# Performance work log

Hardware: AMD Instinct MI355X
Metric: run time of the kernel (lower is better)

The kernel has to match this reference:

```python
import jax, jax.numpy as jnp
import numpy as np

N = 50000
E = 800000
FEAT, ACT = 96, 32
HID, HEADS = 64, 4
NEG_SLOPE = 0.2


def gat_conv(x, src, dst, W, att_s, att_d, bias):
    # x: [N, F_in]; W: [F_in, H*C]; att_s/att_d: [H, C]; bias: [H*C]
    H, C = att_s.shape
    h = (x @ W).reshape(-1, H, C)                      # [N, H, C]
    a_s = jnp.einsum('nhc,hc->nh', h, att_s)           # [N, H]
    a_d = jnp.einsum('nhc,hc->nh', h, att_d)
    e = jax.nn.leaky_relu(a_s[src] + a_d[dst], NEG_SLOPE)  # [E, H]
    m = jax.ops.segment_max(e, dst, num_segments=N)
    e = jnp.exp(e - m[dst])
    denom = jax.ops.segment_sum(e, dst, num_segments=N)
    alpha = e / (denom[dst] + 1e-16)                   # softmax over incoming edges
    out = jax.ops.segment_sum(alpha[:, :, None] * h[src], dst, num_segments=N)
    return out.reshape(-1, H * C) + bias


def setup_inputs() -> dict:
    key = jax.random.key(0)
    ks = jax.random.split(key, 12)
    node_features = jax.random.normal(ks[0], (N, FEAT), dtype=jnp.float32)
    actions = jax.random.normal(ks[1], (N, ACT), dtype=jnp.float32)
    edge_index = jax.random.randint(ks[2], (2, E), 0, N, dtype=jnp.int64)
    s = 0.1
    return {
        'node_features': node_features,
        'actions': actions,
        'edge_index': edge_index,
        'W_emb': jax.random.normal(ks[3], (FEAT + ACT, HID), dtype=jnp.float32) * s,
        'b_emb': jnp.zeros((HID,), dtype=jnp.float32),
        'W1': jax.random.normal(ks[4], (HID, HEADS * HID), dtype=jnp.float32) * s,
        'att_s1': jax.random.normal(ks[5], (HEADS, HID), dtype=jnp.float32) * s,
        'att_d1': jax.random.normal(ks[6], (HEADS, HID), dtype=jnp.float32) * s,
        'b1': jnp.zeros((HEADS * HID,), dtype=jnp.float32),
        'W2': jax.random.normal(ks[7], (HEADS * HID, HID), dtype=jnp.float32) * s,
        'att_s2': jax.random.normal(ks[8], (1, HID), dtype=jnp.float32) * s,
        'att_d2': jax.random.normal(ks[9], (1, HID), dtype=jnp.float32) * s,
        'b2': jnp.zeros((HID,), dtype=jnp.float32),
        'W_v': jax.random.normal(ks[10], (HID, 1), dtype=jnp.float32) * s,
        'b_v': jnp.zeros((1,), dtype=jnp.float32),
    }


def reference(node_features, actions, edge_index, W_emb, b_emb, W1, att_s1, att_d1, b1,
              W2, att_s2, att_d2, b2, W_v, b_v):
    # add self loops (PyG GATConv default add_self_loops=True)
    loop = jnp.arange(N, dtype=edge_index.dtype)
    src = jnp.concatenate([edge_index[0], loop])
    dst = jnp.concatenate([edge_index[1], loop])
    x = jnp.concatenate([node_features, actions], axis=1)
    x = x @ W_emb + b_emb
    x = jax.nn.relu(gat_conv(x, src, dst, W1, att_s1, att_d1, b1))
    x = jax.nn.relu(gat_conv(x, src, dst, W2, att_s2, att_d2, b2))
    g = jnp.mean(x, axis=0, keepdims=True)  # [1, HID]
    return g @ W_v + b_v                    # [1, 1]
```

## Files before the change

kernel.cpp:

```cpp
#include <hip/hip_runtime.h>
#include <hip/hip_bf16.h>
#include <math.h>

#define FEAT 96
#define ACTF 32

using frag8 = __attribute__((ext_vector_type(8))) short;
using f32x4 = __attribute__((ext_vector_type(4))) float;

__device__ __forceinline__ float lrelu(float x) { return x >= 0.f ? x : 0.2f * x; }
__device__ __forceinline__ void atomAddF(float* p, float v) {
    __hip_atomic_fetch_add(p, v, __ATOMIC_RELAXED, __HIP_MEMORY_SCOPE_AGENT);
}
__device__ __forceinline__ float expc(float x) { return __expf(fminf(x, 60.f)); }
__device__ __forceinline__ unsigned short f2bf(float f) {
    __hip_bfloat16 h = __float2bfloat16(f);
    return *(unsigned short*)&h;
}
__device__ __forceinline__ float bf2f(unsigned short u) {
    return __uint_as_float((unsigned)u << 16);
}
__device__ __forceinline__ float bflo(unsigned u) { return __uint_as_float(u << 16); }
__device__ __forceinline__ float bfhi(unsigned u) { return __uint_as_float(u & 0xffff0000u); }

__global__ __launch_bounds__(256) void prep_all(
    const float* __restrict__ nf, const float* __restrict__ act,
    unsigned short* __restrict__ Xh, unsigned short* __restrict__ Xl,
    long long xtot, int xb,
    const float* __restrict__ Wemb, const float* __restrict__ bemb,
    const float* __restrict__ W1,
    unsigned short* __restrict__ wfh, unsigned short* __restrict__ wfl,
    float* __restrict__ bfused,
    const float* __restrict__ W2, __hip_bfloat16* __restrict__ w2t) {
    int b = blockIdx.x;
    if (b < xb) {
        long long i = (long long)b * 256 + threadIdx.x;
        if (i < xtot) {
            int n = (int)(i >> 7), k = (int)(i & 127);
            float v = (k < FEAT) ? nf[(size_t)n * FEAT + k] : act[(size_t)n * ACTF + (k - FEAT)];
            unsigned short h = f2bf(v);
            Xh[i] = h;
            Xl[i] = f2bf(v - bf2f(h));
        }
        return;
    }
    b -= xb;
    if (b < 129) {
        int k = b, c = threadIdx.x;
        if (k < 128) {
            float s = 0.f;
            for (int j = 0; j < 64; ++j) s = fmaf(Wemb[k * 64 + j], W1[j * 256 + c], s);
            unsigned short h = f2bf(s);
            wfh[(size_t)c * 128 + k] = h;
            wfl[(size_t)c * 128 + k] = f2bf(s - bf2f(h));
        } else {
            float s = 0.f;
            for (int j = 0; j < 64; ++j) s = fmaf(bemb[j], W1[j * 256 + c], s);
            bfused[c] = s;
        }
        return;
    }
    b -= 129;
    int i = b * 256 + threadIdx.x;
    int k = i >> 6, c = i & 63;
    w2t[(size_t)c * 256 + k] = __float2bfloat16(W2[i]);
}

__global__ __launch_bounds__(256, 2) void gemm1_hist(
    const unsigned short* __restrict__ Xh, const unsigned short* __restrict__ Xl,
    const unsigned short* __restrict__ wfh, const unsigned short* __restrict__ wfl,
    const float* __restrict__ bfused, const float* __restrict__ att_s,
    const float* __restrict__ att_d, __hip_bfloat16* __restrict__ h1b,
    float* __restrict__ a_s, float* __restrict__ a_d, int N,
    const int* __restrict__ dstp, int* __restrict__ cnt, int E, int ET, int gb) {
    if (blockIdx.x >= gb) {
        int e = (blockIdx.x - gb) * 256 + threadIdx.x;
        if (e < ET) {
            int d = (e < E) ? dstp[e] : (e - E);
            atomicAdd(&cnt[d], 1);
        }
        return;
    }
    int w = threadIdx.x >> 6, l = threadIdx.x & 63;
    int r16 = l & 15, kg = l >> 4;
    frag8 bh[4][4], bl[4][4];
    #pragma unroll
    for (int c = 0; c < 4; ++c) {
        int ct = w * 4 + c;
        const short* bhp = (const short*)wfh + (size_t)(ct * 16 + r16) * 128 + kg * 8;
        const short* blp = (const short*)wfl + (size_t)(ct * 16 + r16) * 128 + kg * 8;
        #pragma unroll
        for (int ks = 0; ks < 4; ++ks) {
            bh[c][ks] = *(const frag8*)(bhp + ks * 32);
            bl[c][ks] = *(const frag8*)(blp + ks * 32);
        }
    }
    float biasv[4], awv[4], dwv[4];
    #pragma unroll
    for (int c = 0; c < 4; ++c) {
        int ch = w * 64 + c * 16 + r16;
        biasv[c] = bfused[ch];
        awv[c] = att_s[ch];
        dwv[c] = att_d[ch];
    }
    int ntiles = (N + 15) >> 4;
    for (int tile = blockIdx.x; tile < ntiles; tile += gb) {
        int nb = tile * 16;
        int arow = nb + r16; if (arow >= N) arow = N - 1;
        const short* ahp = (const short*)Xh + (size_t)arow * 128 + kg * 8;
        const short* alp = (const short*)Xl + (size_t)arow * 128 + kg * 8;
        frag8 ah[4], al[4];
        #pragma unroll
        for (int ks = 0; ks < 4; ++ks) {
            ah[ks] = *(const frag8*)(ahp + ks * 32);
            al[ks] = *(const frag8*)(alp + ks * 32);
        }
        float s_s[4] = {0.f, 0.f, 0.f, 0.f}, s_d[4] = {0.f, 0.f, 0.f, 0.f};
        #pragma unroll
        for (int c = 0; c < 4; ++c) {
            f32x4 acc = (f32x4){0.f, 0.f, 0.f, 0.f};
            #pragma unroll
            for (int ks = 0; ks < 4; ++ks) {
                acc = __builtin_amdgcn_mfma_f32_16x16x32_bf16(ah[ks], bh[c][ks], acc, 0, 0, 0);
                acc = __builtin_amdgcn_mfma_f32_16x16x32_bf16(al[ks], bh[c][ks], acc, 0, 0, 0);
                acc = __builtin_amdgcn_mfma_f32_16x16x32_bf16(ah[ks], bl[c][ks], acc, 0, 0, 0);
            }
            int ch = w * 64 + c * 16 + r16;
            #pragma unroll
            for (int r = 0; r < 4; ++r) {
                int node = nb + kg * 4 + r;
                float v = acc[r] + biasv[c];
                if (node < N) h1b[(size_t)node * 256 + ch] = __float2bfloat16(v);
                s_s[r] = fmaf(v, awv[c], s_s[r]);
                s_d[r] = fmaf(v, dwv[c], s_d[r]);
            }
        }
        #pragma unroll
        for (int r = 0; r < 4; ++r) {
            float vs = s_s[r], vd = s_d[r];
            #pragma unroll
            for (int o = 1; o < 16; o <<= 1) {
                vs += __shfl_xor(vs, o);
                vd += __shfl_xor(vd, o);
            }
            int node = nb + kg * 4 + r;
            if (r16 == 0 && node < N) {
                a_s[(size_t)node * 4 + w] = vs;
                a_d[(size_t)node * 4 + w] = vd;
            }
        }
    }
}

__global__ __launch_bounds__(256, 2) void gemm2_mfma_w(
    const __hip_bfloat16* __restrict__ out1b, const __hip_bfloat16* __restrict__ w2t,
    const float* __restrict__ att_s, const float* __restrict__ att_d,
    __hip_bfloat16* __restrict__ h2b, float* __restrict__ a_s, float* __restrict__ a_d,
    int N) {
    int w = threadIdx.x >> 6, l = threadIdx.x & 63;
    int r16 = l & 15, kg = l >> 4;
    const short* B = (const short*)w2t;
    frag8 b[4][8];
    #pragma unroll
    for (int ct = 0; ct < 4; ++ct) {
        const short* brp = B + (size_t)(ct * 16 + r16) * 256 + kg * 8;
        #pragma unroll
        for (int ks = 0; ks < 8; ++ks)
            b[ct][ks] = *(const frag8*)(brp + ks * 32);
    }
    float awv[4], dwv[4];
    #pragma unroll
    for (int ct = 0; ct < 4; ++ct) {
        int ch = ct * 16 + r16;
        awv[ct] = att_s[ch];
        dwv[ct] = att_d[ch];
    }
    const short* A = (const short*)out1b;
    int ntiles = (N + 15) >> 4;
    for (int tile = blockIdx.x * 4 + w; tile < ntiles; tile += gridDim.x * 4) {
        int nb = tile * 16;
        int arow = nb + r16; if (arow >= N) arow = N - 1;
        const short* arp = A + (size_t)arow * 256 + kg * 8;
        frag8 a[8];
        #pragma unroll
        for (int ks = 0; ks < 8; ++ks) a[ks] = *(const frag8*)(arp + ks * 32);
        float s_s[4] = {0.f, 0.f, 0.f, 0.f}, s_d[4] = {0.f, 0.f, 0.f, 0.f};
        #pragma unroll
        for (int ct = 0; ct < 4; ++ct) {
            f32x4 acc = (f32x4){0.f, 0.f, 0.f, 0.f};
            #pragma unroll
            for (int ks = 0; ks < 8; ++ks)
                acc = __builtin_amdgcn_mfma_f32_16x16x32_bf16(a[ks], b[ct][ks], acc, 0, 0, 0);
            int ch = ct * 16 + r16;
            #pragma unroll
            for (int r = 0; r < 4; ++r) {
                int node = nb + kg * 4 + r;
                float v = acc[r];
                if (node < N) h2b[(size_t)node * 64 + ch] = __float2bfloat16(v);
                s_s[r] = fmaf(v, awv[ct], s_s[r]);
                s_d[r] = fmaf(v, dwv[ct], s_d[r]);
            }
        }
        #pragma unroll
        for (int r = 0; r < 4; ++r) {
            #pragma unroll
            for (int o = 1; o < 16; o <<= 1) {
                s_s[r] += __shfl_xor(s_s[r], o);
                s_d[r] += __shfl_xor(s_d[r], o);
            }
            int node = nb + kg * 4 + r;
            if (r16 == 0 && node < N) { a_s[node] = s_s[r]; a_d[node] = s_d[r]; }
        }
    }
}

__global__ __launch_bounds__(256) void scan_blocks(
    const int* __restrict__ cnt, int* __restrict__ offl, int* __restrict__ bsum, int n) {
    int b = blockIdx.x, t = threadIdx.x;
    int i = b * 256 + t;
    int v = (i < n) ? cnt[i] : 0;
    int lane = t & 63, w = t >> 6;
    int x = v;
    #pragma unroll
    for (int o = 1; o < 64; o <<= 1) {
        int y = __shfl_up(x, o);
        if (lane >= o) x += y;
    }
    __shared__ int wtot[4];
    if (lane == 63) wtot[w] = x;
    __syncthreads();
    int add = 0;
    #pragma unroll
    for (int j = 0; j < 4; ++j) if (j < w) add += wtot[j];
    int incl = x + add;
    if (i < n) offl[i] = incl - v;
    if (t == 255) bsum[b] = incl;
}

__global__ __launch_bounds__(256) void scan_tops(
    const int* __restrict__ bsum, int* __restrict__ bpre, int nb,
    float* __restrict__ g, int* __restrict__ done) {
    int t = threadIdx.x;
    int v = (t < nb) ? bsum[t] : 0;
    int lane = t & 63, w = t >> 6;
    int x = v;
    #pragma unroll
    for (int o = 1; o < 64; o <<= 1) {
        int y = __shfl_up(x, o);
        if (lane >= o) x += y;
    }
    __shared__ int wtot[4];
    if (lane == 63) wtot[w] = x;
    __syncthreads();
    int add = 0;
    #pragma unroll
    for (int j = 0; j < 4; ++j) if (j < w) add += wtot[j];
    if (t < nb) bpre[t] = x + add - v;
    if (t == 255) bpre[nb] = x + add;
    if (t < 64) g[t] = 0.f;
    if (t == 64) *done = 0;
}

__global__ void scatter_fin(const int* __restrict__ src, const int* __restrict__ dst,
                            const int* __restrict__ offl, const int* __restrict__ bpre,
                            int* __restrict__ cur, int* __restrict__ perm,
                            int* __restrict__ off, int E, int ET, int n, int nb, int sb) {
    if (blockIdx.x < sb) {
        int e = blockIdx.x * 256 + threadIdx.x;
        if (e >= ET) return;
        int s = (e < E) ? src[e] : (e - E);
        int d = (e < E) ? dst[e] : (e - E);
        int r = atomicAdd(&cur[d], 1);
        perm[offl[d] + bpre[d >> 8] + r] = s;
    } else {
        int i = (blockIdx.x - sb) * 256 + threadIdx.x;
        if (i < n) off[i] = offl[i] + bpre[i >> 8];
        if (i == n) off[n] = bpre[nb];
    }
}

__global__ __launch_bounds__(256) void fused_gat4(
    const int* __restrict__ off, const int* __restrict__ perm,
    const float* __restrict__ a_s, const float* __restrict__ a_d,
    const __hip_bfloat16* __restrict__ h1b, const float* __restrict__ bias,
    __hip_bfloat16* __restrict__ out1b, int N) {
    __shared__ float exls[4][4][68];
    __shared__ unsigned idxls[4][64];
    int w = threadIdx.x >> 6, l = threadIdx.x & 63;
    int d = blockIdx.x * 4 + w;
    if (d >= N) return;
    int lo = off[d], hi = off[d + 1];
    const float4* as4 = (const float4*)a_s;
    float4 ad = ((const float4*)a_d)[d];
    int eg = l >> 5;
    int li = l & 31;
    int gh = li >> 3;
    const char* hb = (const char*)h1b;
    unsigned laneoff = (unsigned)li * 16u;
    float acc[8] = {0.f, 0.f, 0.f, 0.f, 0.f, 0.f, 0.f, 0.f};
    float dx = 0.f, dy = 0.f, dz = 0.f, dw = 0.f;
    for (int base = lo; base < hi; base += 64) {
        int e = base + l;
        bool valid = e < hi;
        int s = valid ? perm[e] : 0;
        float4 a = as4[s];
        float e0 = valid ? expc(lrelu(a.x + ad.x)) : 0.f;
        float e1 = valid ? expc(lrelu(a.y + ad.y)) : 0.f;
        float e2 = valid ? expc(lrelu(a.z + ad.z)) : 0.f;
        float e3 = valid ? expc(lrelu(a.w + ad.w)) : 0.f;
        dx += e0; dy += e1; dz += e2; dw += e3;
        exls[w][0][l] = e0;
        exls[w][1][l] = e1;
        exls[w][2][l] = e2;
        exls[w][3][l] = e3;
        idxls[w][l] = valid ? (unsigned)s * 512u : 0u;
        int n = min(64, hi - base);
        #pragma unroll 2
        for (int i = 0; i < n; i += 2) {
            int ii = i + eg;
            float ex = exls[w][gh][ii];
            unsigned voff = idxls[w][ii] + laneoff;
            uint4 v = *(const uint4*)(hb + voff);
            acc[0] = fmaf(ex, bflo(v.x), acc[0]);
            acc[1] = fmaf(ex, bfhi(v.x), acc[1]);
            acc[2] = fmaf(ex, bflo(v.y), acc[2]);
            acc[3] = fmaf(ex, bfhi(v.y), acc[3]);
            acc[4] = fmaf(ex, bflo(v.z), acc[4]);
            acc[5] = fmaf(ex, bfhi(v.z), acc[5]);
            acc[6] = fmaf(ex, bflo(v.w), acc[6]);
            acc[7] = fmaf(ex, bfhi(v.w), acc[7]);
        }
    }
    #pragma unroll
    for (int o = 32; o; o >>= 1) {
        dx += __shfl_xor(dx, o); dy += __shfl_xor(dy, o);
        dz += __shfl_xor(dz, o); dw += __shfl_xor(dw, o);
    }
    float rr = 1.f / ((gh == 0 ? dx : gh == 1 ? dy : gh == 2 ? dz : dw) + 1e-16f);
    #pragma unroll
    for (int j = 0; j < 8; ++j) acc[j] += __shfl_xor(acc[j], 32);
    if (eg == 0) {
        float4 b0 = ((const float4*)bias)[li * 2];
        float4 b1 = ((const float4*)bias)[li * 2 + 1];
        uint4 pk;
        pk.x = (unsigned)f2bf(fmaxf(fmaf(acc[0], rr, b0.x), 0.f))
             | ((unsigned)f2bf(fmaxf(fmaf(acc[1], rr, b0.y), 0.f)) << 16);
        pk.y = (unsigned)f2bf(fmaxf(fmaf(acc[2], rr, b0.z), 0.f))
             | ((unsigned)f2bf(fmaxf(fmaf(acc[3], rr, b0.w), 0.f)) << 16);
        pk.z = (unsigned)f2bf(fmaxf(fmaf(acc[4], rr, b1.x), 0.f))
             | ((unsigned)f2bf(fmaxf(fmaf(acc[5], rr, b1.y), 0.f)) << 16);
        pk.w = (unsigned)f2bf(fmaxf(fmaf(acc[6], rr, b1.z), 0.f))
             | ((unsigned)f2bf(fmaxf(fmaf(acc[7], rr, b1.w), 0.f)) << 16);
        ((uint4*)(out1b + (size_t)d * 256))[li] = pk;
    }
}

__global__ __launch_bounds__(256) void fused_gat1(
    const int* __restrict__ off, const int* __restrict__ perm,
    const float* __restrict__ a_s, const float* __restrict__ a_d,
    const __hip_bfloat16* __restrict__ h2b, const float* __restrict__ bias,
    float* __restrict__ out2, int N) {
    __shared__ float exls1[4][64];
    __shared__ unsigned idxls1[4][64];
    int w = threadIdx.x >> 6, l = threadIdx.x & 63;
    int d = blockIdx.x * 4 + w;
    if (d >= N) return;
    int lo = off[d], hi = off[d + 1];
    float add = a_d[d];
    int eg = l >> 4;
    int li = l & 15;
    const char* hb = (const char*)h2b;
    unsigned laneoff = (unsigned)li * 8u;
    float den = 0.f;
    float acc0 = 0.f, acc1 = 0.f, acc2 = 0.f, acc3 = 0.f;
    for (int base = lo; base < hi; base += 64) {
        int e = base + l;
        bool valid = e < hi;
        int s = valid ? perm[e] : 0;
        float ex = valid ? expc(lrelu(a_s[s] + add)) : 0.f;
        den += ex;
        exls1[w][l] = ex;
        idxls1[w][l] = valid ? (unsigned)s * 128u : 0u;
        int n = min(64, hi - base);
        #pragma unroll 4
        for (int i = 0; i < n; i += 4) {
            int ii = i + eg;
            float exx = exls1[w][ii];
            unsigned voff = idxls1[w][ii] + laneoff;
            uint2 v = *(const uint2*)(hb + voff);
            acc0 = fmaf(exx, bflo(v.x), acc0);
            acc1 = fmaf(exx, bfhi(v.x), acc1);
            acc2 = fmaf(exx, bflo(v.y), acc2);
            acc3 = fmaf(exx, bfhi(v.y), acc3);
        }
    }
    #pragma unroll
    for (int o = 32; o; o >>= 1) den += __shfl_xor(den, o);
    float rr = 1.f / (den + 1e-16f);
    #pragma unroll
    for (int o = 16; o < 64; o <<= 1) {
        acc0 += __shfl_xor(acc0, o);
        acc1 += __shfl_xor(acc1, o);
        acc2 += __shfl_xor(acc2, o);
        acc3 += __shfl_xor(acc3, o);
    }
    if (eg == 0 && (l >> 4) == 0) {
        const float4* b4 = (const float4*)bias;
        float4 bv = b4[li];
        float4 o4;
        o4.x = fmaxf(fmaf(acc0, rr, bv.x), 0.f);
        o4.y = fmaxf(fmaf(acc1, rr, bv.y), 0.f);
        o4.z = fmaxf(fmaf(acc2, rr, bv.z), 0.f);
        o4.w = fmaxf(fmaf(acc3, rr, bv.w), 0.f);
        ((float4*)(out2 + (size_t)d * 64))[li] = o4;
    }
}

__global__ __launch_bounds__(256) void colsum_final(
    const float* __restrict__ x, float* __restrict__ g, int* __restrict__ done,
    const float* __restrict__ Wv, const float* __restrict__ bv,
    float* __restrict__ out, int N) {
    __shared__ float part[4][64];
    __shared__ int amlast;
    int c = threadIdx.x & 63;
    int r = threadIdx.x >> 6;
    float acc = 0.f;
    for (long long n = (long long)blockIdx.x * 4 + r; n < N; n += (long long)gridDim.x * 4)
        acc += x[n * 64 + c];
    part[r][c] = acc;
    __syncthreads();
    if (r == 0) {
        float v = part[0][c] + part[1][c] + part[2][c] + part[3][c];
        atomAddF(&g[c], v);
    }
    __threadfence();
    if (threadIdx.x == 0) {
        int t = __hip_atomic_fetch_add(done, 1, __ATOMIC_ACQ_REL, __HIP_MEMORY_SCOPE_AGENT);
        amlast = (t == (int)gridDim.x - 1) ? 1 : 0;
    }
    __syncthreads();
    if (amlast && threadIdx.x < 64) {
        float gc = __hip_atomic_load(&g[threadIdx.x], __ATOMIC_RELAXED, __HIP_MEMORY_SCOPE_AGENT);
        float v = (gc / (float)N) * Wv[threadIdx.x];
        #pragma unroll
        for (int o = 32; o; o >>= 1) v += __shfl_down(v, o);
        if (threadIdx.x == 0) out[0] = v + bv[0];
    }
}

extern "C" void kernel_launch(void* const* d_in, const int* in_sizes, int n_in,
                              void* d_out, int out_size, void* d_ws, size_t ws_size,
                              hipStream_t stream) {
    const float* nf   = (const float*)d_in[0];
    const float* act  = (const float*)d_in[1];
    const int*   ei   = (const int*)d_in[2];
    const float* Wemb = (const float*)d_in[3];
    const float* bemb = (const float*)d_in[4];
    const float* W1   = (const float*)d_in[5];
    const float* as1  = (const float*)d_in[6];
    const float* ad1  = (const float*)d_in[7];
    const float* b1   = (const float*)d_in[8];
    const float* W2   = (const float*)d_in[9];
    const float* as2  = (const float*)d_in[10];
    const float* ad2  = (const float*)d_in[11];
    const float* b2   = (const float*)d_in[12];
    const float* Wv   = (const float*)d_in[13];
    const float* bv   = (const float*)d_in[14];
    float* out = (float*)d_out;

    const int N = in_sizes[0] / FEAT;
    const int E = in_sizes[2] / 2;
    const int ET = E + N;
    const int* srcp = ei;
    const int* dstp = ei + E;
    const int NB = (N + 255) / 256;
    const int HB = (ET + 255) / 256;

    char* ws = (char*)d_ws;
    unsigned short* Xh = (unsigned short*)ws;
    unsigned short* Xl = Xh + (size_t)N * 128;
    __hip_bfloat16* h1b   = (__hip_bfloat16*)(Xl + (size_t)N * 128);
    __hip_bfloat16* out1b = h1b + (size_t)N * 256;
    float* a_s  = (float*)(out1b + (size_t)N * 256);
    float* a_d  = a_s + (size_t)N * 4;
    __hip_bfloat16* h2b = (__hip_bfloat16*)(a_d + (size_t)N * 4);
    float* out2 = (float*)(h2b + (size_t)N * 64);
    float* g    = out2 + (size_t)N * 64;
    __hip_bfloat16* w2t = (__hip_bfloat16*)(g + 64);
    unsigned short* wfh = (unsigned short*)(w2t + 64 * 256);
    unsigned short* wfl = wfh + 256 * 128;
    float* bfused = (float*)(wfl + 256 * 128);
    int* cnt  = (int*)(bfused + 256);
    int* cur  = cnt + N;
    int* offl = cur + N;
    int* off  = offl + N;
    int* perm = off + N + 1;
    int* bsum = perm + ET;
    int* bpre = bsum + NB;
    int* done = bpre + NB + 1;

    (void)ws_size; (void)n_in; (void)out_size;

    hipMemsetAsync(cnt, 0, (size_t)2 * N * sizeof(int), stream);

    long long xtot = (long long)N * 128;
    const int XB = (int)((xtot + 255) / 256);
    prep_all<<<XB + 129 + 64, 256, 0, stream>>>(nf, act, Xh, Xl, xtot, XB,
                                                Wemb, bemb, W1, wfh, wfl, bfused,
                                                W2, w2t);

    const int GB = 1024;
    gemm1_hist<<<GB + HB, 256, 0, stream>>>(Xh, Xl, wfh, wfl, bfused,
                                            as1, ad1, h1b, a_s, a_d, N,
                                            dstp, cnt, E, ET, GB);

    scan_blocks<<<NB, 256, 0, stream>>>(cnt, offl, bsum, N);
    scan_tops<<<1, 256, 0, stream>>>(bsum, bpre, NB, g, done);
    {
        const int FB = (N + 1 + 255) / 256;
        scatter_fin<<<HB + FB, 256, 0, stream>>>(srcp, dstp, offl, bpre, cur,
                                                 perm, off, E, ET, N, NB, HB);
    }

    fused_gat4<<<(N + 3) / 4, 256, 0, stream>>>(off, perm, a_s, a_d, h1b, b1, out1b, N);

    gemm2_mfma_w<<<512, 256, 0, stream>>>(out1b, w2t, as2, ad2, h2b, a_s, a_d, N);
    fused_gat1<<<(N + 3) / 4, 256, 0, stream>>>(off, perm, a_s, a_d, h2b, b2, out2, N);

    colsum_final<<<512, 256, 0, stream>>>(out2, g, done, Wv, bv, out, N);
}
```

Before: 286.4 us.

## Vectorize input bf16 split, prefetch next A tile, split histogram from GEMM1

The input prep now has each thread load 8 floats with float4 reads and write packed uint4 hi/lo bf16 values, replacing scalar per-element loads and stores. GEMM1 software-prefetches the next tile's A fragments into registers while computing the current tile, to hide global load latency. The destination histogram moves out of the fused GEMM kernel into its own launch. That adds one kernel launch and loses any overlap between the two, and the prefetch raises register pressure under launch_bounds(256,2).

```diff
diff --git a/kernel.cpp b/kernel.cpp
--- a/kernel.cpp
+++ b/kernel.cpp
@@ -26,7 +26,7 @@
 __global__ __launch_bounds__(256) void prep_all(
     const float* __restrict__ nf, const float* __restrict__ act,
     unsigned short* __restrict__ Xh, unsigned short* __restrict__ Xl,
-    long long xtot, int xb,
+    int N, int xb,
     const float* __restrict__ Wemb, const float* __restrict__ bemb,
     const float* __restrict__ W1,
     unsigned short* __restrict__ wfh, unsigned short* __restrict__ wfl,
@@ -34,13 +34,34 @@
     const float* __restrict__ W2, __hip_bfloat16* __restrict__ w2t) {
     int b = blockIdx.x;
     if (b < xb) {
-        long long i = (long long)b * 256 + threadIdx.x;
-        if (i < xtot) {
-            int n = (int)(i >> 7), k = (int)(i & 127);
-            float v = (k < FEAT) ? nf[(size_t)n * FEAT + k] : act[(size_t)n * ACTF + (k - FEAT)];
-            unsigned short h = f2bf(v);
-            Xh[i] = h;
-            Xl[i] = f2bf(v - bf2f(h));
+        int gid = b * 256 + threadIdx.x;
+        int node = gid >> 4, sub = gid & 15;
+        if (node < N) {
+            int k0 = sub * 8;
+            float4 v0, v1;
+            if (k0 < FEAT) {
+                const float4* p = (const float4*)(nf + (size_t)node * FEAT + k0);
+                v0 = p[0]; v1 = p[1];
+            } else {
+                const float4* p = (const float4*)(act + (size_t)node * ACTF + (k0 - FEAT));
+                v0 = p[0]; v1 = p[1];
+            }
+            float vv[8] = {v0.x, v0.y, v0.z, v0.w, v1.x, v1.y, v1.z, v1.w};
+            uint4 ph, pl;
+            unsigned hs[8], ls[8];
+            #pragma unroll
+            for (int j = 0; j < 8; ++j) {
+                unsigned short h = f2bf(vv[j]);
+                hs[j] = h;
+                ls[j] = f2bf(vv[j] - bf2f(h));
+            }
+            ph.x = hs[0] | (hs[1] << 16); ph.y = hs[2] | (hs[3] << 16);
+            ph.z = hs[4] | (hs[5] << 16); ph.w = hs[6] | (hs[7] << 16);
+            pl.x = ls[0] | (ls[1] << 16); pl.y = ls[2] | (ls[3] << 16);
+            pl.z = ls[4] | (ls[5] << 16); pl.w = ls[6] | (ls[7] << 16);
+            size_t idx = (size_t)node * 128 + k0;
+            *(uint4*)(Xh + idx) = ph;
+            *(uint4*)(Xl + idx) = pl;
         }
         return;
     }
@@ -66,21 +87,19 @@
     w2t[(size_t)c * 256 + k] = __float2bfloat16(W2[i]);
 }
 
-__global__ __launch_bounds__(256, 2) void gemm1_hist(
+__global__ void hist_kernel(const int* __restrict__ dst, int* __restrict__ cnt, int E, int ET) {
+    int e = blockIdx.x * blockDim.x + threadIdx.x;
+    if (e >= ET) return;
+    int d = (e < E) ? dst[e] : (e - E);
+    atomicAdd(&cnt[d], 1);
+}
+
+__global__ __launch_bounds__(256, 2) void gemm1_mfma_w(
     const unsigned short* __restrict__ Xh, const unsigned short* __restrict__ Xl,
     const unsigned short* __restrict__ wfh, const unsigned short* __restrict__ wfl,
     const float* __restrict__ bfused, const float* __restrict__ att_s,
     const float* __restrict__ att_d, __hip_bfloat16* __restrict__ h1b,
-    float* __restrict__ a_s, float* __restrict__ a_d, int N,
-    const int* __restrict__ dstp, int* __restrict__ cnt, int E, int ET, int gb) {
-    if (blockIdx.x >= gb) {
-        int e = (blockIdx.x - gb) * 256 + threadIdx.x;
-        if (e < ET) {
-            int d = (e < E) ? dstp[e] : (e - E);
-            atomicAdd(&cnt[d], 1);
-        }
-        return;
-    }
+    float* __restrict__ a_s, float* __restrict__ a_d, int N) {
     int w = threadIdx.x >> 6, l = threadIdx.x & 63;
     int r16 = l & 15, kg = l >> 4;
     frag8 bh[4][4], bl[4][4];
@@ -104,16 +123,32 @@
         dwv[c] = att_d[ch];
     }
     int ntiles = (N + 15) >> 4;
-    for (int tile = blockIdx.x; tile < ntiles; tile += gb) {
-        int nb = tile * 16;
-        int arow = nb + r16; if (arow >= N) arow = N - 1;
+    int tile = blockIdx.x;
+    if (tile >= ntiles) return;
+    frag8 ah[4], al[4];
+    {
+        int arow = tile * 16 + r16; if (arow >= N) arow = N - 1;
         const short* ahp = (const short*)Xh + (size_t)arow * 128 + kg * 8;
         const short* alp = (const short*)Xl + (size_t)arow * 128 + kg * 8;
-        frag8 ah[4], al[4];
         #pragma unroll
         for (int ks = 0; ks < 4; ++ks) {
             ah[ks] = *(const frag8*)(ahp + ks * 32);
             al[ks] = *(const frag8*)(alp + ks * 32);
+        }
+    }
+    for (; tile < ntiles; tile += gridDim.x) {
+        int nb = tile * 16;
+        frag8 nah[4], nal[4];
+        int ntile = tile + gridDim.x;
+        if (ntile < ntiles) {
+            int arow = ntile * 16 + r16; if (arow >= N) arow = N - 1;
+            const short* ahp = (const short*)Xh + (size_t)arow * 128 + kg * 8;
+            const short* alp = (const short*)Xl + (size_t)arow * 128 + kg * 8;
+            #pragma unroll
+            for (int ks = 0; ks < 4; ++ks) {
+                nah[ks] = *(const frag8*)(ahp + ks * 32);
+                nal[ks] = *(const frag8*)(alp + ks * 32);
+            }
         }
         float s_s[4] = {0.f, 0.f, 0.f, 0.f}, s_d[4] = {0.f, 0.f, 0.f, 0.f};
         #pragma unroll
@@ -149,6 +184,8 @@
                 a_d[(size_t)node * 4 + w] = vd;
             }
         }
+        #pragma unroll
+        for (int ks = 0; ks < 4; ++ks) { ah[ks] = nah[ks]; al[ks] = nal[ks]; }
     }
 }
 
@@ -503,16 +540,15 @@
 
     hipMemsetAsync(cnt, 0, (size_t)2 * N * sizeof(int), stream);
 
-    long long xtot = (long long)N * 128;
-    const int XB = (int)((xtot + 255) / 256);
-    prep_all<<<XB + 129 + 64, 256, 0, stream>>>(nf, act, Xh, Xl, xtot, XB,
+    const int XB = ((N * 16) + 255) / 256;
+    prep_all<<<XB + 129 + 64, 256, 0, stream>>>(nf, act, Xh, Xl, N, XB,
                                                 Wemb, bemb, W1, wfh, wfl, bfused,
                                                 W2, w2t);
 
-    const int GB = 1024;
-    gemm1_hist<<<GB + HB, 256, 0, stream>>>(Xh, Xl, wfh, wfl, bfused,
-                                            as1, ad1, h1b, a_s, a_d, N,
-                                            dstp, cnt, E, ET, GB);
+    hist_kernel<<<HB, 256, 0, stream>>>(dstp, cnt, E, ET);
+
+    gemm1_mfma_w<<<1024, 256, 0, stream>>>(Xh, Xl, wfh, wfl, bfused,
+                                           as1, ad1, h1b, a_s, a_d, N);
 
     scan_blocks<<<NB, 256, 0, stream>>>(cnt, offl, bsum, N);
     scan_tops<<<1, 256, 0, stream>>>(bsum, bpre, NB, g, done);
```

Result: slower. 300.8 us (+5.0%).
